# Kernel tuning notes

Measured on AMD Instinct MI355X. Metric: run time of the kernel, lower is better.

The kernel has to match this reference:

```python
import jax, jax.numpy as jnp
import numpy as np

TOP_K = 2

def setup_inputs() -> dict:
    key = jax.random.key(0)
    k1, k2, k3 = jax.random.split(key, 3)
    B, S, H, E = 4, 4096, 4096, 64
    return {
        "hidden_states": jax.random.normal(k1, (B, S, H), dtype=jnp.float32),
        "weight": jax.random.normal(k2, (E, H), dtype=jnp.float32),
        "bias": jax.random.normal(k3, (E,), dtype=jnp.float32),
    }

def reference(hidden_states, weight, bias):
    B, S, H = hidden_states.shape
    E = weight.shape[0]
    x = hidden_states.reshape(-1, H)                      # [N, H]
    router_logits = jnp.einsum('nh,eh->ne', x, weight) + bias  # [N, E]
    routing_weights, selected_experts = jax.lax.top_k(router_logits, TOP_K)
    routing_weights = jax.nn.softmax(routing_weights.astype(jnp.float32), axis=-1).astype(hidden_states.dtype)
    N = x.shape[0]
    rows = jnp.arange(N)[:, None]
    final = jnp.zeros((N, E), dtype=router_logits.dtype).at[rows, selected_experts].set(routing_weights)
    return final.reshape(B, S, E), selected_experts
```

## Files before the change

kernel.cpp:

```cpp
#include <hip/hip_runtime.h>
#include <math.h>


constexpr int E_EXPERTS = 64;
constexpr int H_DIM = 4096;
constexpr int BLOCK = 512;
constexpr int ROWS_B = 64;
constexpr int NPH = 32;
constexpr int KSLICE = 1024;
constexpr int REG_SH = 512;
constexpr int BUFS = 48 * REG_SH;
constexpr int W_ELEMS = E_EXPERTS * H_DIM;

typedef __attribute__((ext_vector_type(8))) short short8;
typedef __attribute__((ext_vector_type(4))) float f32x4;

__device__ __forceinline__ float4 ld4(const float* p) {
  return *reinterpret_cast<const float4*>(p);
}

__device__ __forceinline__ void gload16(const unsigned short* g,
                                        unsigned short* l) {
  __builtin_amdgcn_global_load_lds(
      (const __attribute__((address_space(1))) void*)g,
      (__attribute__((address_space(3))) void*)l, 16, 0, 0);
}

__device__ __forceinline__ unsigned short bf_rne(float x) {
  unsigned u = __builtin_bit_cast(unsigned, x);
  return (unsigned short)((u + 0x7fffu + ((u >> 16) & 1u)) >> 16);
}
__device__ __forceinline__ float bf2f(unsigned short b) {
  return __builtin_bit_cast(float, ((unsigned)b) << 16);
}
__device__ __forceinline__ void split3(float x, unsigned short& h,
                                       unsigned short& m, unsigned short& l) {
  unsigned short hb = (unsigned short)(__builtin_bit_cast(unsigned, x) >> 16);
  float r1 = x - bf2f(hb);
  unsigned short mb = (unsigned short)(__builtin_bit_cast(unsigned, r1) >> 16);
  float r2 = r1 - bf2f(mb);
  h = hb;
  m = mb;
  l = bf_rne(r2);
}
__device__ __forceinline__ void split3_8(float4 a, float4 b, short8& h,
                                         short8& m, short8& l) {
  unsigned short hh, mm, ll;
  split3(a.x, hh, mm, ll); h[0] = (short)hh; m[0] = (short)mm; l[0] = (short)ll;
  split3(a.y, hh, mm, ll); h[1] = (short)hh; m[1] = (short)mm; l[1] = (short)ll;
  split3(a.z, hh, mm, ll); h[2] = (short)hh; m[2] = (short)mm; l[2] = (short)ll;
  split3(a.w, hh, mm, ll); h[3] = (short)hh; m[3] = (short)mm; l[3] = (short)ll;
  split3(b.x, hh, mm, ll); h[4] = (short)hh; m[4] = (short)mm; l[4] = (short)ll;
  split3(b.y, hh, mm, ll); h[5] = (short)hh; m[5] = (short)mm; l[5] = (short)ll;
  split3(b.z, hh, mm, ll); h[6] = (short)hh; m[6] = (short)mm; l[6] = (short)ll;
  split3(b.w, hh, mm, ll); h[7] = (short)hh; m[7] = (short)mm; l[7] = (short)ll;
}

__global__ __launch_bounds__(256) void split_w_kernel(
    const float* __restrict__ w, unsigned short* __restrict__ wh,
    unsigned short* __restrict__ wm, unsigned short* __restrict__ wl) {
  const int i = (blockIdx.x * 256 + threadIdx.x) * 4;
  float4 v = ld4(w + i);
  ushort4 h4, m4, l4;
  split3(v.x, h4.x, m4.x, l4.x);
  split3(v.y, h4.y, m4.y, l4.y);
  split3(v.z, h4.z, m4.z, l4.z);
  split3(v.w, h4.w, m4.w, l4.w);
  *reinterpret_cast<ushort4*>(wh + i) = h4;
  *reinterpret_cast<ushort4*>(wm + i) = m4;
  *reinterpret_cast<ushort4*>(wl + i) = l4;
}

__global__ __launch_bounds__(BLOCK, 1) void topk_router_mfma(
    const float* __restrict__ x, const unsigned short* __restrict__ wh,
    const unsigned short* __restrict__ wm,
    const unsigned short* __restrict__ wl, const float* __restrict__ bias,
    float* __restrict__ out_final, float* __restrict__ out_idx) {
  __shared__ unsigned short smem_s[2 * BUFS];

  const int tid = threadIdx.x;
  const int lane = tid & 63;
  const int wid = tid >> 6;
  const int kq = wid & 3;
  const int rh = wid >> 2;
  const int rowBase = blockIdx.x * ROWS_B;
  const int lr = lane & 15;
  const int kg = lane >> 4;

#define DECL_RG(i)                                                       \
  const int r##i = wid * 6 + (i);                                        \
  const int q##i = r##i >> 2;                                            \
  const int rkq##i = q##i / 3;                                           \
  const int rpl##i = q##i - rkq##i * 3;                                  \
  const unsigned short* gb##i =                                          \
      (rpl##i == 0 ? wh : (rpl##i == 1 ? wm : wl)) +                     \
      (size_t)((r##i & 3) * 16 + lr) * H_DIM + rkq##i * KSLICE + kg * 8; \
  unsigned short* lb##i = &smem_s[r##i * REG_SH];
  DECL_RG(0) DECL_RG(1) DECL_RG(2) DECL_RG(3) DECL_RG(4) DECL_RG(5)

#define STAGE(t, buf)                                  \
  do {                                                 \
    gload16(gb0 + (size_t)(t) * 32, lb0 + (buf)*BUFS); \
    gload16(gb1 + (size_t)(t) * 32, lb1 + (buf)*BUFS); \
    gload16(gb2 + (size_t)(t) * 32, lb2 + (buf)*BUFS); \
    gload16(gb3 + (size_t)(t) * 32, lb3 + (buf)*BUFS); \
    gload16(gb4 + (size_t)(t) * 32, lb4 + (buf)*BUFS); \
    gload16(gb5 + (size_t)(t) * 32, lb5 + (buf)*BUFS); \
  } while (0)

  const float* __restrict__ xr0 =
      x + (size_t)(rowBase + rh * 32 + lr) * H_DIM + kq * KSLICE + kg * 8;
  const float* __restrict__ xr1 = xr0 + (size_t)16 * H_DIM;

  float4 xA0, xA1, xA2, xA3, xB0, xB1, xB2, xB3;
#define XLOADA(t)                          \
  do {                                     \
    xA0 = ld4(xr0 + (size_t)(t) * 32);     \
    xA1 = ld4(xr0 + (size_t)(t) * 32 + 4); \
    xA2 = ld4(xr1 + (size_t)(t) * 32);     \
    xA3 = ld4(xr1 + (size_t)(t) * 32 + 4); \
  } while (0)
#define XLOADB(t)                          \
  do {                                     \
    xB0 = ld4(xr0 + (size_t)(t) * 32);     \
    xB1 = ld4(xr0 + (size_t)(t) * 32 + 4); \
    xB2 = ld4(xr1 + (size_t)(t) * 32);     \
    xB3 = ld4(xr1 + (size_t)(t) * 32 + 4); \
  } while (0)

  f32x4 accA0 = {0.f, 0.f, 0.f, 0.f}, accA1 = accA0, accA2 = accA0,
        accA3 = accA0, accB0 = accA0, accB1 = accA0, accB2 = accA0,
        accB3 = accA0;

  STAGE(0, 0);
  __builtin_amdgcn_sched_barrier(0);
  XLOADA(0);
  XLOADB(1);
  asm volatile("s_waitcnt vmcnt(0)" ::: "memory");
  __builtin_amdgcn_s_barrier();
  __builtin_amdgcn_sched_barrier(0);

#define FRAG(buf, eg, pl)                                                  \
  (*reinterpret_cast<const short8*>(                                       \
      &smem_s[(size_t)(buf)*BUFS + ((kq * 3 + (pl)) * 4 + (eg)) * REG_SH + \
              lane * 8]))

#define MM(d, a, b) d = __builtin_amdgcn_mfma_f32_16x16x32_bf16(a, b, d, 0, 0, 0)
#define PROD6(d, Ah, Am, Al, Bh, Bm, Bl)                      \
  MM(d, Ah, Bh); MM(d, Ah, Bm); MM(d, Am, Bh); MM(d, Am, Bm); \
  MM(d, Ah, Bl); MM(d, Al, Bh)

#define PHASE(p, buf, X0, X1, X2, X3, XLOADM)                           \
  do {                                                                  \
    if ((p) + 1 < NPH) STAGE((p) + 1, (buf) ^ 1);   \
    __builtin_amdgcn_sched_barrier(0);     \
    short8 b0h = FRAG(buf, 0, 0), b0m = FRAG(buf, 0, 1),                \
           b0l = FRAG(buf, 0, 2);                                       \
    short8 b1h = FRAG(buf, 1, 0), b1m = FRAG(buf, 1, 1),                \
           b1l = FRAG(buf, 1, 2);                                       \
    short8 b2h = FRAG(buf, 2, 0), b2m = FRAG(buf, 2, 1),                \
           b2l = FRAG(buf, 2, 2);                                       \
    short8 b3h = FRAG(buf, 3, 0), b3m = FRAG(buf, 3, 1),                \
           b3l = FRAG(buf, 3, 2);                                       \
    short8 ah0, am0, al0, ah1, am1, al1;                                \
    split3_8(X0, X1, ah0, am0, al0);            \
    split3_8(X2, X3, ah1, am1, al1);                                    \
    if ((p) + 2 < NPH) XLOADM((p) + 2);  \
    PROD6(accA0, ah0, am0, al0, b0h, b0m, b0l);                         \
    PROD6(accA1, ah0, am0, al0, b1h, b1m, b1l);                         \
    PROD6(accA2, ah0, am0, al0, b2h, b2m, b2l);                         \
    PROD6(accA3, ah0, am0, al0, b3h, b3m, b3l);                         \
    PROD6(accB0, ah1, am1, al1, b0h, b0m, b0l);                         \
    PROD6(accB1, ah1, am1, al1, b1h, b1m, b1l);                         \
    PROD6(accB2, ah1, am1, al1, b2h, b2m, b2l);                         \
    PROD6(accB3, ah1, am1, al1, b3h, b3m, b3l);                         \
    if ((p) + 2 < NPH) {                                                \
      asm volatile("s_waitcnt vmcnt(4)" ::: "memory");  \
    } else {                                                            \
      asm volatile("s_waitcnt vmcnt(0)" ::: "memory");  \
    }                                                                   \
    __builtin_amdgcn_s_barrier();                                       \
    __builtin_amdgcn_sched_barrier(0);                                  \
  } while (0)

  for (int p = 0; p < NPH; p += 2) {
    PHASE(p, 0, xA0, xA1, xA2, xA3, XLOADA);
    PHASE(p + 1, 1, xB0, xB1, xB2, xB3, XLOADB);
  }

  float* part = reinterpret_cast<float*>(smem_s);
  const int pr = kg * 4;
  const int rwA = rh * 32 + pr;
  const int rwB = rh * 32 + 16 + pr;
#define PSTORE(A, rw, g)                                        \
  part[(size_t)(kq * 64 + (rw) + 0) * 68 + (g)*16 + lr] = A[0]; \
  part[(size_t)(kq * 64 + (rw) + 1) * 68 + (g)*16 + lr] = A[1]; \
  part[(size_t)(kq * 64 + (rw) + 2) * 68 + (g)*16 + lr] = A[2]; \
  part[(size_t)(kq * 64 + (rw) + 3) * 68 + (g)*16 + lr] = A[3];
  PSTORE(accA0, rwA, 0)
  PSTORE(accA1, rwA, 1)
  PSTORE(accA2, rwA, 2)
  PSTORE(accA3, rwA, 3)
  PSTORE(accB0, rwB, 0)
  PSTORE(accB1, rwB, 1)
  PSTORE(accB2, rwB, 2)
  PSTORE(accB3, rwB, 3)
  asm volatile("s_waitcnt lgkmcnt(0)" ::: "memory");
  __builtin_amdgcn_s_barrier();

  const int r = tid >> 3;
  const int eb = (tid & 7) * 8;
  const int n = rowBase + r;

  float v8[8];
#pragma unroll
  for (int j = 0; j < 8; ++j) {
    int e = eb + j;
    v8[j] = ((part[(size_t)(0 * 64 + r) * 68 + e] +
              part[(size_t)(1 * 64 + r) * 68 + e]) +
             (part[(size_t)(2 * 64 + r) * 68 + e] +
              part[(size_t)(3 * 64 + r) * 68 + e])) +
            bias[e];
  }

  float av = -INFINITY, bv = -INFINITY;
  int ai = E_EXPERTS, bi = E_EXPERTS;
#pragma unroll
  for (int j = 0; j < 8; ++j) {
    int e = eb + j;
    float v = v8[j];
    bool beats_a = (v > av) || (v == av && e < ai);
    bool beats_b = (v > bv) || (v == bv && e < bi);
    if (beats_a) {
      bv = av; bi = ai; av = v; ai = e;
    } else if (beats_b) {
      bv = v; bi = e;
    }
  }
#pragma unroll
  for (int d = 1; d < 8; d <<= 1) {
    float av2 = __shfl_xor(av, d);
    float bv2 = __shfl_xor(bv, d);
    int ai2 = __shfl_xor(ai, d);
    int bi2 = __shfl_xor(bi, d);
    bool afirst = (av > av2) || (av == av2 && ai < ai2);
    float na, nb;
    int nai, nbi;
    if (afirst) {
      na = av; nai = ai;
      bool t = (bv > av2) || (bv == av2 && bi < ai2);
      nb = t ? bv : av2;
      nbi = t ? bi : ai2;
    } else {
      na = av2; nai = ai2;
      bool t = (av > bv2) || (av == bv2 && ai < bi2);
      nb = t ? av : bv2;
      nbi = t ? ai : bi2;
    }
    av = na; ai = nai; bv = nb; bi = nbi;
  }

  float e1 = expf(bv - av);
  float denom = 1.0f + e1;
  float p0 = 1.0f / denom;
  float p1 = e1 / denom;

#pragma unroll
  for (int i = 0; i < 2; ++i) {
    float4 o4;
    float* po = &o4.x;
#pragma unroll
    for (int j = 0; j < 4; ++j) {
      int e = eb + i * 4 + j;
      po[j] = (e == ai) ? p0 : (e == bi) ? p1 : 0.0f;
    }
    *reinterpret_cast<float4*>(&out_final[(size_t)n * E_EXPERTS + eb + i * 4]) =
        o4;
  }
  if ((tid & 7) == 0) {
    out_idx[(size_t)n * 2 + 0] = (float)ai;
    out_idx[(size_t)n * 2 + 1] = (float)bi;
  }
}

extern "C" void kernel_launch(void* const* d_in, const int* in_sizes, int n_in,
                              void* d_out, int out_size, void* d_ws,
                              size_t ws_size, hipStream_t stream) {
  const float* x = (const float*)d_in[0];
  const float* w = (const float*)d_in[1];
  const float* bias = (const float*)d_in[2];
  const int N = in_sizes[0] / H_DIM;
  float* out_final = (float*)d_out;
  float* out_idx = out_final + (size_t)N * E_EXPERTS;

  unsigned short* wh = (unsigned short*)d_ws;
  unsigned short* wm = wh + W_ELEMS;
  unsigned short* wl = wm + W_ELEMS;

  split_w_kernel<<<W_ELEMS / (256 * 4), 256, 0, stream>>>(w, wh, wm, wl);
  topk_router_mfma<<<N / ROWS_B, BLOCK, 0, stream>>>(x, wh, wm, wl, bias,
                                                     out_final, out_idx);
}
```

Before: 92.08 us.

## Halve block to 256 threads and 32 rows, split K in two for occupancy

Reworks the router GEMM tiling so each block handles 32 rows with 4 waves: two row groups of 16 and two K-halves of 2048, instead of 64 rows with 8 waves over four K-quarters. Each wave now holds one row tile with four accumulators, LDS staging shrinks to 24 regions per buffer, and launch bounds request two blocks per CU. The aim is more resident blocks and less register and LDS pressure per block, so global-load latency is hidden better. In exchange, each weight fragment loaded into LDS is reused over half as many rows, so weight traffic per output row doubles. The phase loop is also twice as long.

```diff
diff --git a/kernel.cpp b/kernel.cpp
--- a/kernel.cpp
+++ b/kernel.cpp
@@ -4,12 +4,13 @@
 
 constexpr int E_EXPERTS = 64;
 constexpr int H_DIM = 4096;
-constexpr int BLOCK = 512;
-constexpr int ROWS_B = 64;
-constexpr int NPH = 32;
-constexpr int KSLICE = 1024;
+constexpr int BLOCK = 256;
+constexpr int ROWS_B = 32;
+constexpr int NPH = 64;
+constexpr int KSLICE = 2048;
 constexpr int REG_SH = 512;
-constexpr int BUFS = 48 * REG_SH;
+constexpr int NREG = 24;
+constexpr int BUFS = NREG * REG_SH;
 constexpr int W_ELEMS = E_EXPERTS * H_DIM;
 
 typedef __attribute__((ext_vector_type(8))) short short8;
@@ -71,7 +72,7 @@
   *reinterpret_cast<ushort4*>(wl + i) = l4;
 }
 
-__global__ __launch_bounds__(BLOCK, 1) void topk_router_mfma(
+__global__ __launch_bounds__(BLOCK, 2) void topk_router_mfma(
     const float* __restrict__ x, const unsigned short* __restrict__ wh,
     const unsigned short* __restrict__ wm,
     const unsigned short* __restrict__ wl, const float* __restrict__ bias,
@@ -81,8 +82,8 @@
   const int tid = threadIdx.x;
   const int lane = tid & 63;
   const int wid = tid >> 6;
-  const int kq = wid & 3;
-  const int rh = wid >> 2;
+  const int kq = wid & 1;
+  const int rh = wid >> 1;
   const int rowBase = blockIdx.x * ROWS_B;
   const int lr = lane & 15;
   const int kg = lane >> 4;
@@ -109,28 +110,21 @@
   } while (0)
 
   const float* __restrict__ xr0 =
-      x + (size_t)(rowBase + rh * 32 + lr) * H_DIM + kq * KSLICE + kg * 8;
-  const float* __restrict__ xr1 = xr0 + (size_t)16 * H_DIM;
-
-  float4 xA0, xA1, xA2, xA3, xB0, xB1, xB2, xB3;
+      x + (size_t)(rowBase + rh * 16 + lr) * H_DIM + kq * KSLICE + kg * 8;
+
+  float4 xA0, xA1, xB0, xB1;
 #define XLOADA(t)                          \
   do {                                     \
     xA0 = ld4(xr0 + (size_t)(t) * 32);     \
     xA1 = ld4(xr0 + (size_t)(t) * 32 + 4); \
-    xA2 = ld4(xr1 + (size_t)(t) * 32);     \
-    xA3 = ld4(xr1 + (size_t)(t) * 32 + 4); \
   } while (0)
 #define XLOADB(t)                          \
   do {                                     \
     xB0 = ld4(xr0 + (size_t)(t) * 32);     \
     xB1 = ld4(xr0 + (size_t)(t) * 32 + 4); \
-    xB2 = ld4(xr1 + (size_t)(t) * 32);     \
-    xB3 = ld4(xr1 + (size_t)(t) * 32 + 4); \
-  } while (0)
-
-  f32x4 accA0 = {0.f, 0.f, 0.f, 0.f}, accA1 = accA0, accA2 = accA0,
-        accA3 = accA0, accB0 = accA0, accB1 = accA0, accB2 = accA0,
-        accB3 = accA0;
+  } while (0)
+
+  f32x4 acc0 = {0.f, 0.f, 0.f, 0.f}, acc1 = acc0, acc2 = acc0, acc3 = acc0;
 
   STAGE(0, 0);
   __builtin_amdgcn_sched_barrier(0);
@@ -150,7 +144,7 @@
   MM(d, Ah, Bh); MM(d, Ah, Bm); MM(d, Am, Bh); MM(d, Am, Bm); \
   MM(d, Ah, Bl); MM(d, Al, Bh)
 
-#define PHASE(p, buf, X0, X1, X2, X3, XLOADM)                           \
+#define PHASE(p, buf, X0, X1, XLOADM)                                   \
   do {                                                                  \
     if ((p) + 1 < NPH) STAGE((p) + 1, (buf) ^ 1);   \
     __builtin_amdgcn_sched_barrier(0);     \
@@ -162,20 +156,15 @@
            b2l = FRAG(buf, 2, 2);                                       \
     short8 b3h = FRAG(buf, 3, 0), b3m = FRAG(buf, 3, 1),                \
            b3l = FRAG(buf, 3, 2);                                       \
-    short8 ah0, am0, al0, ah1, am1, al1;                                \
-    split3_8(X0, X1, ah0, am0, al0);            \
-    split3_8(X2, X3, ah1, am1, al1);                                    \
+    short8 ah, am, al;                                                  \
+    split3_8(X0, X1, ah, am, al);               \
     if ((p) + 2 < NPH) XLOADM((p) + 2);  \
-    PROD6(accA0, ah0, am0, al0, b0h, b0m, b0l);                         \
-    PROD6(accA1, ah0, am0, al0, b1h, b1m, b1l);                         \
-    PROD6(accA2, ah0, am0, al0, b2h, b2m, b2l);                         \
-    PROD6(accA3, ah0, am0, al0, b3h, b3m, b3l);                         \
-    PROD6(accB0, ah1, am1, al1, b0h, b0m, b0l);                         \
-    PROD6(accB1, ah1, am1, al1, b1h, b1m, b1l);                         \
-    PROD6(accB2, ah1, am1, al1, b2h, b2m, b2l);                         \
-    PROD6(accB3, ah1, am1, al1, b3h, b3m, b3l);                         \
+    PROD6(acc0, ah, am, al, b0h, b0m, b0l);                             \
+    PROD6(acc1, ah, am, al, b1h, b1m, b1l);                             \
+    PROD6(acc2, ah, am, al, b2h, b2m, b2l);                             \
+    PROD6(acc3, ah, am, al, b3h, b3m, b3l);                             \
     if ((p) + 2 < NPH) {                                                \
-      asm volatile("s_waitcnt vmcnt(4)" ::: "memory");  \
+      asm volatile("s_waitcnt vmcnt(2)" ::: "memory");  \
     } else {                                                            \
       asm volatile("s_waitcnt vmcnt(0)" ::: "memory");  \
     }                                                                   \
@@ -184,27 +173,21 @@
   } while (0)
 
   for (int p = 0; p < NPH; p += 2) {
-    PHASE(p, 0, xA0, xA1, xA2, xA3, XLOADA);
-    PHASE(p + 1, 1, xB0, xB1, xB2, xB3, XLOADB);
+    PHASE(p, 0, xA0, xA1, XLOADA);
+    PHASE(p + 1, 1, xB0, xB1, XLOADB);
   }
 
   float* part = reinterpret_cast<float*>(smem_s);
-  const int pr = kg * 4;
-  const int rwA = rh * 32 + pr;
-  const int rwB = rh * 32 + 16 + pr;
-#define PSTORE(A, rw, g)                                        \
-  part[(size_t)(kq * 64 + (rw) + 0) * 68 + (g)*16 + lr] = A[0]; \
-  part[(size_t)(kq * 64 + (rw) + 1) * 68 + (g)*16 + lr] = A[1]; \
-  part[(size_t)(kq * 64 + (rw) + 2) * 68 + (g)*16 + lr] = A[2]; \
-  part[(size_t)(kq * 64 + (rw) + 3) * 68 + (g)*16 + lr] = A[3];
-  PSTORE(accA0, rwA, 0)
-  PSTORE(accA1, rwA, 1)
-  PSTORE(accA2, rwA, 2)
-  PSTORE(accA3, rwA, 3)
-  PSTORE(accB0, rwB, 0)
-  PSTORE(accB1, rwB, 1)
-  PSTORE(accB2, rwB, 2)
-  PSTORE(accB3, rwB, 3)
+  const int pr = rh * 16 + kg * 4;
+#define PSTORE(A, g)                                      \
+  part[(size_t)(kq * 32 + pr + 0) * 68 + (g)*16 + lr] = A[0]; \
+  part[(size_t)(kq * 32 + pr + 1) * 68 + (g)*16 + lr] = A[1]; \
+  part[(size_t)(kq * 32 + pr + 2) * 68 + (g)*16 + lr] = A[2]; \
+  part[(size_t)(kq * 32 + pr + 3) * 68 + (g)*16 + lr] = A[3];
+  PSTORE(acc0, 0)
+  PSTORE(acc1, 1)
+  PSTORE(acc2, 2)
+  PSTORE(acc3, 3)
   asm volatile("s_waitcnt lgkmcnt(0)" ::: "memory");
   __builtin_amdgcn_s_barrier();
 
@@ -216,10 +199,8 @@
 #pragma unroll
   for (int j = 0; j < 8; ++j) {
     int e = eb + j;
-    v8[j] = ((part[(size_t)(0 * 64 + r) * 68 + e] +
-              part[(size_t)(1 * 64 + r) * 68 + e]) +
-             (part[(size_t)(2 * 64 + r) * 68 + e] +
-              part[(size_t)(3 * 64 + r) * 68 + e])) +
+    v8[j] = (part[(size_t)(0 * 32 + r) * 68 + e] +
+             part[(size_t)(1 * 32 + r) * 68 + e]) +
             bias[e];
   }
 
```

Result: slower. 136.9 us (+48.7%).

## Load split weight fragments directly into registers instead of staging through LDS

Applied to the files above, without the earlier changes.

Replaces the double-buffered global-to-LDS staging of the three bf16 weight planes with direct per-lane global loads into registers, double-buffered in software across two register sets. Shared memory shrinks to the reduction scratch, and launch bounds allow two blocks per CU. This removes the LDS round trip and the per-phase barriers. In exchange it raises register pressure considerably and sends redundant weight reads from every wave to L2/L1 instead of sharing one staged copy per block.

```diff
diff --git a/kernel.cpp b/kernel.cpp
--- a/kernel.cpp
+++ b/kernel.cpp
@@ -6,10 +6,8 @@
 constexpr int H_DIM = 4096;
 constexpr int BLOCK = 512;
 constexpr int ROWS_B = 64;
-constexpr int NPH = 32;
 constexpr int KSLICE = 1024;
-constexpr int REG_SH = 512;
-constexpr int BUFS = 48 * REG_SH;
+constexpr int NCH = 32;
 constexpr int W_ELEMS = E_EXPERTS * H_DIM;
 
 typedef __attribute__((ext_vector_type(8))) short short8;
@@ -18,12 +16,8 @@
 __device__ __forceinline__ float4 ld4(const float* p) {
   return *reinterpret_cast<const float4*>(p);
 }
-
-__device__ __forceinline__ void gload16(const unsigned short* g,
-                                        unsigned short* l) {
-  __builtin_amdgcn_global_load_lds(
-      (const __attribute__((address_space(1))) void*)g,
-      (__attribute__((address_space(3))) void*)l, 16, 0, 0);
+__device__ __forceinline__ short8 lds8(const unsigned short* p) {
+  return *reinterpret_cast<const short8*>(p);
 }
 
 __device__ __forceinline__ unsigned short bf_rne(float x) {
@@ -71,12 +65,12 @@
   *reinterpret_cast<ushort4*>(wl + i) = l4;
 }
 
-__global__ __launch_bounds__(BLOCK, 1) void topk_router_mfma(
+__global__ __launch_bounds__(BLOCK, 2) void topk_router_mfma(
     const float* __restrict__ x, const unsigned short* __restrict__ wh,
     const unsigned short* __restrict__ wm,
     const unsigned short* __restrict__ wl, const float* __restrict__ bias,
     float* __restrict__ out_final, float* __restrict__ out_idx) {
-  __shared__ unsigned short smem_s[2 * BUFS];
+  __shared__ float part[4 * ROWS_B * 68];
 
   const int tid = threadIdx.x;
   const int lane = tid & 63;
@@ -87,30 +81,37 @@
   const int lr = lane & 15;
   const int kg = lane >> 4;
 
-#define DECL_RG(i)                                                       \
-  const int r##i = wid * 6 + (i);                                        \
-  const int q##i = r##i >> 2;                                            \
-  const int rkq##i = q##i / 3;                                           \
-  const int rpl##i = q##i - rkq##i * 3;                                  \
-  const unsigned short* gb##i =                                          \
-      (rpl##i == 0 ? wh : (rpl##i == 1 ? wm : wl)) +                     \
-      (size_t)((r##i & 3) * 16 + lr) * H_DIM + rkq##i * KSLICE + kg * 8; \
-  unsigned short* lb##i = &smem_s[r##i * REG_SH];
-  DECL_RG(0) DECL_RG(1) DECL_RG(2) DECL_RG(3) DECL_RG(4) DECL_RG(5)
-
-#define STAGE(t, buf)                                  \
-  do {                                                 \
-    gload16(gb0 + (size_t)(t) * 32, lb0 + (buf)*BUFS); \
-    gload16(gb1 + (size_t)(t) * 32, lb1 + (buf)*BUFS); \
-    gload16(gb2 + (size_t)(t) * 32, lb2 + (buf)*BUFS); \
-    gload16(gb3 + (size_t)(t) * 32, lb3 + (buf)*BUFS); \
-    gload16(gb4 + (size_t)(t) * 32, lb4 + (buf)*BUFS); \
-    gload16(gb5 + (size_t)(t) * 32, lb5 + (buf)*BUFS); \
-  } while (0)
+  const size_t wo = (size_t)lr * H_DIM + kq * KSLICE + kg * 8;
+  const unsigned short* __restrict__ wh0 = wh + wo;
+  const unsigned short* __restrict__ wh1 = wh0 + (size_t)16 * H_DIM;
+  const unsigned short* __restrict__ wh2 = wh0 + (size_t)32 * H_DIM;
+  const unsigned short* __restrict__ wh3 = wh0 + (size_t)48 * H_DIM;
+  const unsigned short* __restrict__ wm0 = wm + wo;
+  const unsigned short* __restrict__ wm1 = wm0 + (size_t)16 * H_DIM;
+  const unsigned short* __restrict__ wm2 = wm0 + (size_t)32 * H_DIM;
+  const unsigned short* __restrict__ wm3 = wm0 + (size_t)48 * H_DIM;
+  const unsigned short* __restrict__ wl0 = wl + wo;
+  const unsigned short* __restrict__ wl1 = wl0 + (size_t)16 * H_DIM;
+  const unsigned short* __restrict__ wl2 = wl0 + (size_t)32 * H_DIM;
+  const unsigned short* __restrict__ wl3 = wl0 + (size_t)48 * H_DIM;
 
   const float* __restrict__ xr0 =
       x + (size_t)(rowBase + rh * 32 + lr) * H_DIM + kq * KSLICE + kg * 8;
   const float* __restrict__ xr1 = xr0 + (size_t)16 * H_DIM;
+
+  short8 w0h, w1h, w2h, w3h, w0m, w1m, w2m, w3m, w0l, w1l, w2l, w3l;
+  short8 v0h, v1h, v2h, v3h, v0m, v1m, v2m, v3m, v0l, v1l, v2l, v3l;
+
+#define WLOAD(P, t)                                \
+  do {                                             \
+    const size_t o_ = (size_t)(t) * 32;            \
+    P##0h = lds8(wh0 + o_); P##1h = lds8(wh1 + o_); \
+    P##2h = lds8(wh2 + o_); P##3h = lds8(wh3 + o_); \
+    P##0m = lds8(wm0 + o_); P##1m = lds8(wm1 + o_); \
+    P##2m = lds8(wm2 + o_); P##3m = lds8(wm3 + o_); \
+    P##0l = lds8(wl0 + o_); P##1l = lds8(wl1 + o_); \
+    P##2l = lds8(wl2 + o_); P##3l = lds8(wl3 + o_); \
+  } while (0)
 
   float4 xA0, xA1, xA2, xA3, xB0, xB1, xB2, xB3;
 #define XLOADA(t)                          \
@@ -132,63 +133,40 @@
         accA3 = accA0, accB0 = accA0, accB1 = accA0, accB2 = accA0,
         accB3 = accA0;
 
-  STAGE(0, 0);
-  __builtin_amdgcn_sched_barrier(0);
-  XLOADA(0);
-  XLOADB(1);
-  asm volatile("s_waitcnt vmcnt(0)" ::: "memory");
-  __builtin_amdgcn_s_barrier();
-  __builtin_amdgcn_sched_barrier(0);
-
-#define FRAG(buf, eg, pl)                                                  \
-  (*reinterpret_cast<const short8*>(                                       \
-      &smem_s[(size_t)(buf)*BUFS + ((kq * 3 + (pl)) * 4 + (eg)) * REG_SH + \
-              lane * 8]))
-
 #define MM(d, a, b) d = __builtin_amdgcn_mfma_f32_16x16x32_bf16(a, b, d, 0, 0, 0)
 #define PROD6(d, Ah, Am, Al, Bh, Bm, Bl)                      \
   MM(d, Ah, Bh); MM(d, Ah, Bm); MM(d, Am, Bh); MM(d, Am, Bm); \
   MM(d, Ah, Bl); MM(d, Al, Bh)
-
-#define PHASE(p, buf, X0, X1, X2, X3, XLOADM)                           \
-  do {                                                                  \
-    if ((p) + 1 < NPH) STAGE((p) + 1, (buf) ^ 1);   \
-    __builtin_amdgcn_sched_barrier(0);     \
-    short8 b0h = FRAG(buf, 0, 0), b0m = FRAG(buf, 0, 1),                \
-           b0l = FRAG(buf, 0, 2);                                       \
-    short8 b1h = FRAG(buf, 1, 0), b1m = FRAG(buf, 1, 1),                \
-           b1l = FRAG(buf, 1, 2);                                       \
-    short8 b2h = FRAG(buf, 2, 0), b2m = FRAG(buf, 2, 1),                \
-           b2l = FRAG(buf, 2, 2);                                       \
-    short8 b3h = FRAG(buf, 3, 0), b3m = FRAG(buf, 3, 1),                \
-           b3l = FRAG(buf, 3, 2);                                       \
-    short8 ah0, am0, al0, ah1, am1, al1;                                \
-    split3_8(X0, X1, ah0, am0, al0);            \
-    split3_8(X2, X3, ah1, am1, al1);                                    \
-    if ((p) + 2 < NPH) XLOADM((p) + 2);  \
-    PROD6(accA0, ah0, am0, al0, b0h, b0m, b0l);                         \
-    PROD6(accA1, ah0, am0, al0, b1h, b1m, b1l);                         \
-    PROD6(accA2, ah0, am0, al0, b2h, b2m, b2l);                         \
-    PROD6(accA3, ah0, am0, al0, b3h, b3m, b3l);                         \
-    PROD6(accB0, ah1, am1, al1, b0h, b0m, b0l);                         \
-    PROD6(accB1, ah1, am1, al1, b1h, b1m, b1l);                         \
-    PROD6(accB2, ah1, am1, al1, b2h, b2m, b2l);                         \
-    PROD6(accB3, ah1, am1, al1, b3h, b3m, b3l);                         \
-    if ((p) + 2 < NPH) {                                                \
-      asm volatile("s_waitcnt vmcnt(4)" ::: "memory");  \
-    } else {                                                            \
-      asm volatile("s_waitcnt vmcnt(0)" ::: "memory");  \
-    }                                                                   \
-    __builtin_amdgcn_s_barrier();                                       \
-    __builtin_amdgcn_sched_barrier(0);                                  \
-  } while (0)
-
-  for (int p = 0; p < NPH; p += 2) {
-    PHASE(p, 0, xA0, xA1, xA2, xA3, XLOADA);
-    PHASE(p + 1, 1, xB0, xB1, xB2, xB3, XLOADB);
-  }
-
-  float* part = reinterpret_cast<float*>(smem_s);
+#define MFMA48(P, A0h, A0m, A0l, A1h, A1m, A1l)        \
+  do {                                                 \
+    PROD6(accA0, A0h, A0m, A0l, P##0h, P##0m, P##0l);  \
+    PROD6(accA1, A0h, A0m, A0l, P##1h, P##1m, P##1l);  \
+    PROD6(accA2, A0h, A0m, A0l, P##2h, P##2m, P##2l);  \
+    PROD6(accA3, A0h, A0m, A0l, P##3h, P##3m, P##3l);  \
+    PROD6(accB0, A1h, A1m, A1l, P##0h, P##0m, P##0l);  \
+    PROD6(accB1, A1h, A1m, A1l, P##1h, P##1m, P##1l);  \
+    PROD6(accB2, A1h, A1m, A1l, P##2h, P##2m, P##2l);  \
+    PROD6(accB3, A1h, A1m, A1l, P##3h, P##3m, P##3l);  \
+  } while (0)
+
+  WLOAD(w, 0);
+  XLOADA(0);
+  XLOADB(1);
+
+  short8 a0h, a0m, a0l, a1h, a1m, a1l;
+  for (int c = 0; c < NCH; c += 2) {
+    WLOAD(v, c + 1);
+    split3_8(xA0, xA1, a0h, a0m, a0l);
+    split3_8(xA2, xA3, a1h, a1m, a1l);
+    if (c + 2 < NCH) XLOADA(c + 2);
+    MFMA48(w, a0h, a0m, a0l, a1h, a1m, a1l);
+    if (c + 2 < NCH) WLOAD(w, c + 2);
+    split3_8(xB0, xB1, a0h, a0m, a0l);
+    split3_8(xB2, xB3, a1h, a1m, a1l);
+    if (c + 3 < NCH) XLOADB(c + 3);
+    MFMA48(v, a0h, a0m, a0l, a1h, a1m, a1l);
+  }
+
   const int pr = kg * 4;
   const int rwA = rh * 32 + pr;
   const int rwB = rh * 32 + 16 + pr;
@@ -205,8 +183,7 @@
   PSTORE(accB1, rwB, 1)
   PSTORE(accB2, rwB, 2)
   PSTORE(accB3, rwB, 3)
-  asm volatile("s_waitcnt lgkmcnt(0)" ::: "memory");
-  __builtin_amdgcn_s_barrier();
+  __syncthreads();
 
   const int r = tid >> 3;
   const int eb = (tid & 7) * 8;
```

Measured after the change: 133.9 us. 45.4% more time.
